# Kernel tuning notes

Hardware: AMD Instinct MI355X
Metric: run time of the kernel (lower is better)

The kernel has to match this reference:

```python
import jax, jax.numpy as jnp
import numpy as np

N_USER = 200000
N_ITEM = 200000
N_EDGE = 6400000
FEAT = 128
HID = 128
ALPHA = 0.1  # opt['leakey']


def _leaky(x):
    return jnp.where(x >= 0, x, ALPHA * x)


def setup_inputs() -> dict:
    key = jax.random.key(0)
    ks = jax.random.split(key, 16)
    s = 0.05
    return {
        "ufea": jax.random.normal(ks[0], (N_USER, FEAT), jnp.float32),
        "vfea": jax.random.normal(ks[1], (N_ITEM, FEAT), jnp.float32),
        "uv_rows": jax.random.randint(ks[2], (N_EDGE,), 0, N_USER, jnp.int32),
        "uv_cols": jax.random.randint(ks[3], (N_EDGE,), 0, N_ITEM, jnp.int32),
        "uv_vals": jax.random.uniform(ks[4], (N_EDGE,), jnp.float32),
        "vu_vals": jax.random.uniform(ks[5], (N_EDGE,), jnp.float32),
        "W1": jax.random.normal(ks[6], (FEAT, HID), jnp.float32) * s,
        "b1": jnp.zeros((HID,), jnp.float32),
        "W2": jax.random.normal(ks[7], (FEAT, HID), jnp.float32) * s,
        "b2": jnp.zeros((HID,), jnp.float32),
        "W3": jax.random.normal(ks[8], (HID, FEAT), jnp.float32) * s,
        "b3": jnp.zeros((FEAT,), jnp.float32),
        "W4": jax.random.normal(ks[9], (HID, FEAT), jnp.float32) * s,
        "b4": jnp.zeros((FEAT,), jnp.float32),
        "Wu": jax.random.normal(ks[10], (2 * FEAT, FEAT), jnp.float32) * s,
        "bu": jnp.zeros((FEAT,), jnp.float32),
        "Wi": jax.random.normal(ks[11], (2 * FEAT, FEAT), jnp.float32) * s,
        "bi": jnp.zeros((FEAT,), jnp.float32),
    }


def _spmm_u2i(vals, rows, cols, h):
    # VU_adj @ h : out[item] = sum_e vals[e] * h[rows[e]]
    return jax.ops.segment_sum(vals[:, None] * h[rows], cols, num_segments=N_ITEM)


def _spmm_i2u(vals, rows, cols, h):
    # UV_adj @ h : out[user] = sum_e vals[e] * h[cols[e]]
    return jax.ops.segment_sum(vals[:, None] * h[cols], rows, num_segments=N_USER)


def reference(ufea, vfea, uv_rows, uv_cols, uv_vals, vu_vals,
              W1, b1, W2, b2, W3, b3, W4, b4, Wu, bu, Wi, bi):
    # gc1: GCN(feat->hid) with VU_adj : users aggregated onto items
    user_ho = _leaky(_spmm_u2i(vu_vals, uv_rows, uv_cols, ufea @ W1) + b1)
    # gc2: GCN(feat->hid) with UV_adj : items aggregated onto users
    item_ho = _leaky(_spmm_i2u(uv_vals, uv_rows, uv_cols, vfea @ W2) + b2)
    # gc3: GCN(hid->feat) with UV_adj : back to user side
    user_ho = _leaky(_spmm_i2u(uv_vals, uv_rows, uv_cols, user_ho @ W3) + b3)
    # gc4: GCN(hid->feat) with VU_adj : back to item side
    item_ho = _leaky(_spmm_u2i(vu_vals, uv_rows, uv_cols, item_ho @ W4) + b4)
    user = jnp.concatenate([user_ho, ufea], axis=1) @ Wu + bu
    item = jnp.concatenate([item_ho, vfea], axis=1) @ Wi + bi
    return jax.nn.relu(user), jax.nn.relu(item)
```

## Files before the change

kernel.cpp:

```cpp
#include <hip/hip_runtime.h>

#define N_NODE 200000
#define FEAT 128
#define ALPHA 0.1f
#define NB 782
#define P2CAP 9216
#define VQ 16383.0f

typedef __bf16 bf16x8 __attribute__((ext_vector_type(8)));
typedef float  f32x4  __attribute__((ext_vector_type(4)));

__device__ inline unsigned short bf16r(float x) {
    unsigned u = __float_as_uint(x);
    u += ((u >> 16) & 1u) + 0x7FFFu;
    return (unsigned short)(u >> 16);
}
__device__ inline unsigned bf16pk(float a, float b) {
    unsigned ua = __float_as_uint(a); ua += ((ua >> 16) & 1u) + 0x7FFFu;
    unsigned ub = __float_as_uint(b); ub += ((ub >> 16) & 1u) + 0x7FFFu;
    return (ua >> 16) | (ub & 0xFFFF0000u);
}
__device__ inline bf16x8 cvt8(const float* __restrict__ p) {
    float4 a = *(const float4*)p, b = *(const float4*)(p + 4);
    union { bf16x8 v; unsigned short u[8]; } o;
    o.u[0] = bf16r(a.x); o.u[1] = bf16r(a.y); o.u[2] = bf16r(a.z); o.u[3] = bf16r(a.w);
    o.u[4] = bf16r(b.x); o.u[5] = bf16r(b.y); o.u[6] = bf16r(b.z); o.u[7] = bf16r(b.w);
    return o.v;
}

__global__ __launch_bounds__(512) void p0_hist(
        const int* __restrict__ rows, const int* __restrict__ cols,
        int* __restrict__ cntA, int* __restrict__ cntB, int nedge) {
    __shared__ int hA[NB], hB[NB];
    int t = threadIdx.x;
    for (int i = t; i < NB; i += 512) { hA[i] = 0; hB[i] = 0; }
    __syncthreads();
    int b0 = blockIdx.x * 16384;
    int bend = min(b0 + 16384, nedge);
    for (int e = b0 + t; e < bend; e += 512) {
        atomicAdd(&hA[cols[e] >> 8], 1);
        atomicAdd(&hB[rows[e] >> 8], 1);
    }
    __syncthreads();
    for (int i = t; i < NB; i += 512) {
        if (hA[i]) atomicAdd(&cntA[i], hA[i]);
        if (hB[i]) atomicAdd(&cntB[i], hB[i]);
    }
}

__global__ __launch_bounds__(1024) void scan2(
        const int* __restrict__ cntA, const int* __restrict__ cntB,
        int* __restrict__ bBaseA, int* __restrict__ bCurA,
        int* __restrict__ bBaseB, int* __restrict__ bCurB, int nedge) {
    __shared__ int s[1024];
    int t = threadIdx.x;
    for (int pass = 0; pass < 2; ++pass) {
        const int* cnt = pass ? cntB : cntA;
        int* bBase = pass ? bBaseB : bBaseA;
        int* bCur  = pass ? bCurB  : bCurA;
        int v = (t < NB) ? cnt[t] : 0;
        s[t] = v;
        __syncthreads();
        for (int o = 1; o < 1024; o <<= 1) {
            int a = (t >= o) ? s[t - o] : 0;
            __syncthreads();
            s[t] += a;
            __syncthreads();
        }
        int exc = s[t] - v;
        if (t < NB) { bBase[t] = exc; bCur[t] = exc; }
        if (t == 0) bBase[NB] = nedge;
        __syncthreads();
    }
}

#define BIN_E 32768
__global__ __launch_bounds__(512) void bin_dual(
        const int* __restrict__ rows, const int* __restrict__ cols,
        const float* __restrict__ uvv, const float* __restrict__ vuv,
        int* __restrict__ bCurA, int* __restrict__ bCurB,
        int2* __restrict__ sA, int2* __restrict__ sB, int nedge) {
    __shared__ int hA[NB], hB[NB], baA[NB], baB[NB], cuA[NB], cuB[NB];
    int t = threadIdx.x;
    for (int i = t; i < NB; i += 512) { hA[i] = 0; hB[i] = 0; }
    __syncthreads();
    int b0 = blockIdx.x * BIN_E;
    int bend = min(b0 + BIN_E, nedge);
    for (int e = b0 + t; e < bend; e += 512) {
        atomicAdd(&hA[cols[e] >> 8], 1);
        atomicAdd(&hB[rows[e] >> 8], 1);
    }
    __syncthreads();
    for (int i = t; i < NB; i += 512) {
        baA[i] = hA[i] ? atomicAdd(&bCurA[i], hA[i]) : 0;  cuA[i] = 0;
        baB[i] = hB[i] ? atomicAdd(&bCurB[i], hB[i]) : 0;  cuB[i] = 0;
    }
    __syncthreads();
    for (int e = b0 + t; e < bend; e += 512) {
        int r = rows[e], c = cols[e];
        int kA = c >> 8;
        int pA = baA[kA] + atomicAdd(&cuA[kA], 1);
        sA[pA] = make_int2(((c & 255) << 18) | r, __float_as_int(vuv[e]));
        int kB = r >> 8;
        int pB = baB[kB] + atomicAdd(&cuB[kB], 1);
        sB[pB] = make_int2(((r & 255) << 18) | c, __float_as_int(uvv[e]));
    }
}

__global__ __launch_bounds__(512) void p2_sort(
        const int2* __restrict__ sA, const int* __restrict__ bBaseA,
        unsigned* __restrict__ eA, int* __restrict__ rpA,
        const int2* __restrict__ sB, const int* __restrict__ bBaseB,
        unsigned* __restrict__ eB, int* __restrict__ rpB) {
    __shared__ unsigned sorted[P2CAP];
    __shared__ int c256[256], off[256];
    const int2* s; const int* bB; unsigned* e; int* rp;
    if (blockIdx.y == 0) { s = sA; bB = bBaseA; e = eA; rp = rpA; }
    else                 { s = sB; bB = bBaseB; e = eB; rp = rpB; }
    int k = blockIdx.x;
    int base = bB[k], end = bB[k + 1];
    int t = threadIdx.x;
    if (t < 256) c256[t] = 0;
    __syncthreads();
    for (int i = base + t; i < end; i += 512)
        atomicAdd(&c256[((unsigned)s[i].x) >> 18], 1);
    __syncthreads();
    int v = (t < 256) ? c256[t] : 0;
    if (t < 256) off[t] = v;
    __syncthreads();
    for (int o = 1; o < 256; o <<= 1) {
        int a = (t >= o && t < 256) ? off[t - o] : 0;
        __syncthreads();
        if (t < 256) off[t] += a;
        __syncthreads();
    }
    if (t < 256) {
        int exc = off[t] - v;
        off[t] = exc;
        c256[t] = 0;
        int node = (k << 8) + t;
        if (node < N_NODE) rp[node] = base + exc;
    }
    __syncthreads();
    for (int i = base + t; i < end; i += 512) {
        int2 rec = s[i];
        int loc = ((unsigned)rec.x) >> 18;
        int slot = off[loc] + atomicAdd(&c256[loc], 1);
        unsigned q = (unsigned)__float2int_rn(__int_as_float(rec.y) * VQ);
        if (slot < P2CAP)
            sorted[slot] = (((unsigned)rec.x & 0x3FFFFu) << 14) | q;
    }
    __syncthreads();
    int cnt = end - base;
    if (cnt > P2CAP) cnt = P2CAP;
    for (int i = t; i < cnt; i += 512)
        e[base + i] = sorted[i];
    if (k == NB - 1 && t == 0) rp[N_NODE] = bB[NB];
}

__global__ __launch_bounds__(256) void wtrans(
        const float* __restrict__ W, unsigned short* __restrict__ Wt, int K) {
    int idx = blockIdx.x * 256 + threadIdx.x;
    if (idx >= K * 128) return;
    int k = idx >> 7, n = idx & 127;
    Wt[n * K + k] = bf16r(W[idx]);
}

__global__ __launch_bounds__(256) void spmm_gather_act_bf16(
        const unsigned* __restrict__ src, unsigned* __restrict__ dst,
        const int* __restrict__ rp, const unsigned* __restrict__ edges,
        const float* __restrict__ bias, int ndst) {
    int wid = __builtin_amdgcn_readfirstlane(
        (int)((blockIdx.x * 256u + threadIdx.x) >> 6));
    int lane = threadIdx.x & 63;
    if (wid >= ndst) return;
    float2 b = *(const float2*)(bias + lane * 2);
    int e0 = rp[wid], e1 = rp[wid + 1];
    float accx = 0.f, accy = 0.f;
    const float vs = 1.0f / VQ;
    int e = e0;
    for (; e + 8 <= e1; e += 8) {
        unsigned r0 = edges[e],     r1 = edges[e + 1];
        unsigned r2 = edges[e + 2], r3 = edges[e + 3];
        unsigned r4 = edges[e + 4], r5 = edges[e + 5];
        unsigned r6 = edges[e + 6], r7 = edges[e + 7];
        unsigned p0 = src[(size_t)(r0 >> 14) * 64 + lane];
        unsigned p1 = src[(size_t)(r1 >> 14) * 64 + lane];
        unsigned p2 = src[(size_t)(r2 >> 14) * 64 + lane];
        unsigned p3 = src[(size_t)(r3 >> 14) * 64 + lane];
        unsigned p4 = src[(size_t)(r4 >> 14) * 64 + lane];
        unsigned p5 = src[(size_t)(r5 >> 14) * 64 + lane];
        unsigned p6 = src[(size_t)(r6 >> 14) * 64 + lane];
        unsigned p7 = src[(size_t)(r7 >> 14) * 64 + lane];
        float v0 = (float)(r0 & 16383u) * vs, v1 = (float)(r1 & 16383u) * vs;
        float v2 = (float)(r2 & 16383u) * vs, v3 = (float)(r3 & 16383u) * vs;
        float v4 = (float)(r4 & 16383u) * vs, v5 = (float)(r5 & 16383u) * vs;
        float v6 = (float)(r6 & 16383u) * vs, v7 = (float)(r7 & 16383u) * vs;
        accx = fmaf(v0, __uint_as_float(p0 << 16), accx);
        accy = fmaf(v0, __uint_as_float(p0 & 0xFFFF0000u), accy);
        accx = fmaf(v1, __uint_as_float(p1 << 16), accx);
        accy = fmaf(v1, __uint_as_float(p1 & 0xFFFF0000u), accy);
        accx = fmaf(v2, __uint_as_float(p2 << 16), accx);
        accy = fmaf(v2, __uint_as_float(p2 & 0xFFFF0000u), accy);
        accx = fmaf(v3, __uint_as_float(p3 << 16), accx);
        accy = fmaf(v3, __uint_as_float(p3 & 0xFFFF0000u), accy);
        accx = fmaf(v4, __uint_as_float(p4 << 16), accx);
        accy = fmaf(v4, __uint_as_float(p4 & 0xFFFF0000u), accy);
        accx = fmaf(v5, __uint_as_float(p5 << 16), accx);
        accy = fmaf(v5, __uint_as_float(p5 & 0xFFFF0000u), accy);
        accx = fmaf(v6, __uint_as_float(p6 << 16), accx);
        accy = fmaf(v6, __uint_as_float(p6 & 0xFFFF0000u), accy);
        accx = fmaf(v7, __uint_as_float(p7 << 16), accx);
        accy = fmaf(v7, __uint_as_float(p7 & 0xFFFF0000u), accy);
    }
    for (; e < e1; ++e) {
        unsigned r = edges[e];
        unsigned p = src[(size_t)(r >> 14) * 64 + lane];
        float v = (float)(r & 16383u) * vs;
        accx = fmaf(v, __uint_as_float(p << 16), accx);
        accy = fmaf(v, __uint_as_float(p & 0xFFFF0000u), accy);
    }
    float ox = accx + b.x;
    float oy = accy + b.y;
    ox = (ox >= 0.f) ? ox : ALPHA * ox;
    oy = (oy >= 0.f) ? oy : ALPHA * oy;
    dst[(size_t)wid * 64 + lane] = bf16pk(ox, oy);
}

__global__ __launch_bounds__(256) void gemm16(
        const unsigned short* __restrict__ X, const unsigned short* __restrict__ Wt,
        unsigned short* __restrict__ O, int M) {
    int l = threadIdx.x & 63, wv = threadIdx.x >> 6;
    int lr = l & 15, lh = l >> 4;
    int row0 = blockIdx.x * 128 + wv * 32;
    int ra = row0 + lr, rb = row0 + 16 + lr;
    if (ra >= M) ra = M - 1;
    if (rb >= M) rb = M - 1;
    const unsigned short* xa = X + (size_t)ra * 128;
    const unsigned short* xb = X + (size_t)rb * 128;
    f32x4 acc[2][8] = {};
#pragma unroll
    for (int ks = 0; ks < 4; ++ks) {
        int ko = ks * 32 + lh * 8;
        bf16x8 a0 = *(const bf16x8*)(xa + ko);
        bf16x8 a1 = *(const bf16x8*)(xb + ko);
#pragma unroll
        for (int nf = 0; nf < 8; ++nf) {
            bf16x8 b = *(const bf16x8*)(Wt + (nf * 16 + lr) * 128 + ko);
            acc[0][nf] = __builtin_amdgcn_mfma_f32_16x16x32_bf16(a0, b, acc[0][nf], 0, 0, 0);
            acc[1][nf] = __builtin_amdgcn_mfma_f32_16x16x32_bf16(a1, b, acc[1][nf], 0, 0, 0);
        }
    }
#pragma unroll
    for (int half = 0; half < 2; ++half) {
        int orow = row0 + half * 16 + lh * 4;
#pragma unroll
        for (int j = 0; j < 4; ++j) {
            if (orow + j < M) {
                unsigned short* op = O + (size_t)(orow + j) * 128 + lr;
#pragma unroll
                for (int nf = 0; nf < 8; ++nf)
                    op[nf * 16] = bf16r(acc[half][nf][j]);
            }
        }
    }
}

__global__ __launch_bounds__(256) void gemm16_f32(
        const float* __restrict__ Xf, const unsigned short* __restrict__ Wt,
        unsigned short* __restrict__ O, int M) {
    int l = threadIdx.x & 63, wv = threadIdx.x >> 6;
    int lr = l & 15, lh = l >> 4;
    int row0 = blockIdx.x * 128 + wv * 32;
    int ra = row0 + lr, rb = row0 + 16 + lr;
    if (ra >= M) ra = M - 1;
    if (rb >= M) rb = M - 1;
    const float* xa = Xf + (size_t)ra * 128;
    const float* xb = Xf + (size_t)rb * 128;
    f32x4 acc[2][8] = {};
#pragma unroll
    for (int ks = 0; ks < 4; ++ks) {
        int ko = ks * 32 + lh * 8;
        bf16x8 a0 = cvt8(xa + ko);
        bf16x8 a1 = cvt8(xb + ko);
#pragma unroll
        for (int nf = 0; nf < 8; ++nf) {
            bf16x8 b = *(const bf16x8*)(Wt + (nf * 16 + lr) * 128 + ko);
            acc[0][nf] = __builtin_amdgcn_mfma_f32_16x16x32_bf16(a0, b, acc[0][nf], 0, 0, 0);
            acc[1][nf] = __builtin_amdgcn_mfma_f32_16x16x32_bf16(a1, b, acc[1][nf], 0, 0, 0);
        }
    }
#pragma unroll
    for (int half = 0; half < 2; ++half) {
        int orow = row0 + half * 16 + lh * 4;
#pragma unroll
        for (int j = 0; j < 4; ++j) {
            if (orow + j < M) {
                unsigned short* op = O + (size_t)(orow + j) * 128 + lr;
#pragma unroll
                for (int nf = 0; nf < 8; ++nf)
                    op[nf * 16] = bf16r(acc[half][nf][j]);
            }
        }
    }
}

__global__ __launch_bounds__(256) void gemm16_concat(
        const unsigned short* __restrict__ T, const float* __restrict__ F,
        const unsigned short* __restrict__ Wt, const float* __restrict__ bias,
        float* __restrict__ O, int M) {
    int l = threadIdx.x & 63, wv = threadIdx.x >> 6;
    int lr = l & 15, lh = l >> 4;
    int row0 = blockIdx.x * 128 + wv * 32;
    int ra = row0 + lr, rb = row0 + 16 + lr;
    if (ra >= M) ra = M - 1;
    if (rb >= M) rb = M - 1;
    f32x4 acc[2][8] = {};
#pragma unroll
    for (int ks = 0; ks < 8; ++ks) {
        int ko = (ks & 3) * 32 + lh * 8;
        bf16x8 a0, a1;
        if (ks < 4) {
            a0 = *(const bf16x8*)(T + (size_t)ra * 128 + ko);
            a1 = *(const bf16x8*)(T + (size_t)rb * 128 + ko);
        } else {
            a0 = cvt8(F + (size_t)ra * 128 + ko);
            a1 = cvt8(F + (size_t)rb * 128 + ko);
        }
        int wko = ks * 32 + lh * 8;
#pragma unroll
        for (int nf = 0; nf < 8; ++nf) {
            bf16x8 b = *(const bf16x8*)(Wt + (nf * 16 + lr) * 256 + wko);
            acc[0][nf] = __builtin_amdgcn_mfma_f32_16x16x32_bf16(a0, b, acc[0][nf], 0, 0, 0);
            acc[1][nf] = __builtin_amdgcn_mfma_f32_16x16x32_bf16(a1, b, acc[1][nf], 0, 0, 0);
        }
    }
    float bv[8];
#pragma unroll
    for (int nf = 0; nf < 8; ++nf) bv[nf] = bias[nf * 16 + lr];
#pragma unroll
    for (int half = 0; half < 2; ++half) {
        int orow = row0 + half * 16 + lh * 4;
#pragma unroll
        for (int j = 0; j < 4; ++j) {
            if (orow + j < M) {
                float* op = O + (size_t)(orow + j) * 128 + lr;
#pragma unroll
                for (int nf = 0; nf < 8; ++nf) {
                    float v = acc[half][nf][j] + bv[nf];
                    op[nf * 16] = v > 0.f ? v : 0.f;
                }
            }
        }
    }
}

extern "C" void kernel_launch(void* const* d_in, const int* in_sizes, int n_in,
                              void* d_out, int out_size, void* d_ws, size_t ws_size,
                              hipStream_t stream) {
    const float* ufea    = (const float*)d_in[0];
    const float* vfea    = (const float*)d_in[1];
    const int*   uv_rows = (const int*)d_in[2];
    const int*   uv_cols = (const int*)d_in[3];
    const float* uv_vals = (const float*)d_in[4];
    const float* vu_vals = (const float*)d_in[5];
    const float* W1 = (const float*)d_in[6];
    const float* b1 = (const float*)d_in[7];
    const float* W2 = (const float*)d_in[8];
    const float* b2 = (const float*)d_in[9];
    const float* W3 = (const float*)d_in[10];
    const float* b3 = (const float*)d_in[11];
    const float* W4 = (const float*)d_in[12];
    const float* b4 = (const float*)d_in[13];
    const float* Wu = (const float*)d_in[14];
    const float* bu = (const float*)d_in[15];
    const float* Wi = (const float*)d_in[16];
    const float* bi = (const float*)d_in[17];

    float* out_user = (float*)d_out;
    float* out_item = out_user + (size_t)N_NODE * FEAT;

    int nedge = in_sizes[2];
    size_t nfe = (size_t)N_NODE * FEAT;

    unsigned short* G1 = (unsigned short*)d_ws;
    unsigned short* G2 = G1 + nfe;
    unsigned short* Ta = G2 + nfe;
    unsigned short* Tb = Ta + nfe;
    unsigned short* W1t = Tb + nfe;
    unsigned short* W2t = W1t + 128 * 128;
    unsigned short* W3t = W2t + 128 * 128;
    unsigned short* W4t = W3t + 128 * 128;
    unsigned short* Wut = W4t + 128 * 128;
    unsigned short* Wit = Wut + 128 * 256;
    int* rpA    = (int*)(Wit + 128 * 256);
    int* rpB    = rpA + (N_NODE + 64);
    int* cntA   = rpB + (N_NODE + 64);
    int* cntB   = cntA + 1024;
    int* bBaseA = cntB + 1024;
    int* bBaseB = bBaseA + 1024;
    int* bCurA  = bBaseB + 1024;
    int* bCurB  = bCurA + 1024;
    unsigned* eA = (unsigned*)(bCurB + 1024);
    unsigned* eB = eA + nedge;

    int2* sA = (int2*)G1;
    int2* sB = (int2*)G2;

    dim3 b512(512), b256(256);
    int hb  = (nedge + 16383) / 16384;
    int binb = (nedge + BIN_E - 1) / BIN_E;
    dim3 mgrid((unsigned)((N_NODE + 127) / 128));
    dim3 sgrid((unsigned)(N_NODE / 4));
    dim3 p2grid(NB, 2);

    hipMemsetAsync(cntA, 0, 2048 * sizeof(int), stream);
    p0_hist<<<hb, b512, 0, stream>>>(uv_rows, uv_cols, cntA, cntB, nedge);
    scan2<<<1, 1024, 0, stream>>>(cntA, cntB, bBaseA, bCurA, bBaseB, bCurB, nedge);
    bin_dual<<<binb, b512, 0, stream>>>(uv_rows, uv_cols, uv_vals, vu_vals,
                                        bCurA, bCurB, sA, sB, nedge);
    p2_sort<<<p2grid, b512, 0, stream>>>(sA, bBaseA, eA, rpA,
                                         sB, bBaseB, eB, rpB);

    wtrans<<<64, b256, 0, stream>>>(W1, W1t, 128);
    wtrans<<<64, b256, 0, stream>>>(W2, W2t, 128);
    wtrans<<<64, b256, 0, stream>>>(W3, W3t, 128);
    wtrans<<<64, b256, 0, stream>>>(W4, W4t, 128);
    wtrans<<<128, b256, 0, stream>>>(Wu, Wut, 256);
    wtrans<<<128, b256, 0, stream>>>(Wi, Wit, 256);

    gemm16_f32<<<mgrid, b256, 0, stream>>>(ufea, W1t, G1, N_NODE);
    spmm_gather_act_bf16<<<sgrid, b256, 0, stream>>>(
        (const unsigned*)G1, (unsigned*)Ta, rpA, eA, b1, N_NODE);

    gemm16_f32<<<mgrid, b256, 0, stream>>>(vfea, W2t, G2, N_NODE);
    spmm_gather_act_bf16<<<sgrid, b256, 0, stream>>>(
        (const unsigned*)G2, (unsigned*)Tb, rpB, eB, b2, N_NODE);

    gemm16<<<mgrid, b256, 0, stream>>>(Ta, W3t, G1, N_NODE);
    spmm_gather_act_bf16<<<sgrid, b256, 0, stream>>>(
        (const unsigned*)G1, (unsigned*)Ta, rpB, eB, b3, N_NODE);

    gemm16<<<mgrid, b256, 0, stream>>>(Tb, W4t, G2, N_NODE);
    spmm_gather_act_bf16<<<sgrid, b256, 0, stream>>>(
        (const unsigned*)G2, (unsigned*)Tb, rpA, eA, b4, N_NODE);

    gemm16_concat<<<mgrid, b256, 0, stream>>>(Ta, ufea, Wut, bu, out_user, N_NODE);
    gemm16_concat<<<mgrid, b256, 0, stream>>>(Tb, vfea, Wit, bi, out_item, N_NODE);
}
```

Before: 1.600 ms.

## Fuse per-bucket local sort into SpMM gather, dropping CSR build pass

Removes the separate p2_sort kernel and the compact CSR edge arrays. Each SpMM launch now loads its bucket's binned records, counting-sorts them in shared memory and immediately does the weighted gather with bias and leaky ReLU. Binned records get dedicated workspace, and the binning kernel switches to a fixed count of 128 blocks. This saves a global write and read of sorted edges, but repeats the sort in every SpMM, reads wider records, and runs far fewer, longer-lived waves.

Result: slower. 1.761 ms (+10.1%).

```diff
diff --git a/kernel.cpp b/kernel.cpp
--- a/kernel.cpp
+++ b/kernel.cpp
@@ -4,7 +4,7 @@
 #define FEAT 128
 #define ALPHA 0.1f
 #define NB 782
-#define P2CAP 9216
+#define GCAP 9216
 #define VQ 16383.0f
 
 typedef __bf16 bf16x8 __attribute__((ext_vector_type(8)));
@@ -74,18 +74,18 @@
     }
 }
 
-#define BIN_E 32768
 __global__ __launch_bounds__(512) void bin_dual(
         const int* __restrict__ rows, const int* __restrict__ cols,
         const float* __restrict__ uvv, const float* __restrict__ vuv,
         int* __restrict__ bCurA, int* __restrict__ bCurB,
-        int2* __restrict__ sA, int2* __restrict__ sB, int nedge) {
+        int2* __restrict__ sA, int2* __restrict__ sB,
+        int nedge, int chunk) {
     __shared__ int hA[NB], hB[NB], baA[NB], baB[NB], cuA[NB], cuB[NB];
     int t = threadIdx.x;
     for (int i = t; i < NB; i += 512) { hA[i] = 0; hB[i] = 0; }
     __syncthreads();
-    int b0 = blockIdx.x * BIN_E;
-    int bend = min(b0 + BIN_E, nedge);
+    int b0 = blockIdx.x * chunk;
+    int bend = min(b0 + chunk, nedge);
     for (int e = b0 + t; e < bend; e += 512) {
         atomicAdd(&hA[cols[e] >> 8], 1);
         atomicAdd(&hB[rows[e] >> 8], 1);
@@ -107,25 +107,21 @@
     }
 }
 
-__global__ __launch_bounds__(512) void p2_sort(
-        const int2* __restrict__ sA, const int* __restrict__ bBaseA,
-        unsigned* __restrict__ eA, int* __restrict__ rpA,
-        const int2* __restrict__ sB, const int* __restrict__ bBaseB,
-        unsigned* __restrict__ eB, int* __restrict__ rpB) {
-    __shared__ unsigned sorted[P2CAP];
-    __shared__ int c256[256], off[256];
-    const int2* s; const int* bB; unsigned* e; int* rp;
-    if (blockIdx.y == 0) { s = sA; bB = bBaseA; e = eA; rp = rpA; }
-    else                 { s = sB; bB = bBaseB; e = eB; rp = rpB; }
+__global__ __launch_bounds__(512) void bucket_gather(
+        const int2* __restrict__ recs, const int* __restrict__ bBase,
+        const unsigned* __restrict__ G, unsigned* __restrict__ dstF,
+        const float* __restrict__ bias) {
+    __shared__ unsigned sorted[GCAP];
+    __shared__ int cnt[256], off[256];
     int k = blockIdx.x;
-    int base = bB[k], end = bB[k + 1];
+    int base = bBase[k], end = bBase[k + 1];
     int t = threadIdx.x;
-    if (t < 256) c256[t] = 0;
+    if (t < 256) cnt[t] = 0;
     __syncthreads();
     for (int i = base + t; i < end; i += 512)
-        atomicAdd(&c256[((unsigned)s[i].x) >> 18], 1);
-    __syncthreads();
-    int v = (t < 256) ? c256[t] : 0;
+        atomicAdd(&cnt[((unsigned)recs[i].x) >> 18], 1);
+    __syncthreads();
+    int v = (t < 256) ? cnt[t] : 0;
     if (t < 256) off[t] = v;
     __syncthreads();
     for (int o = 1; o < 256; o <<= 1) {
@@ -134,28 +130,61 @@
         if (t < 256) off[t] += a;
         __syncthreads();
     }
-    if (t < 256) {
-        int exc = off[t] - v;
-        off[t] = exc;
-        c256[t] = 0;
-        int node = (k << 8) + t;
-        if (node < N_NODE) rp[node] = base + exc;
-    }
+    if (t < 256) { off[t] -= v; cnt[t] = 0; }
     __syncthreads();
     for (int i = base + t; i < end; i += 512) {
-        int2 rec = s[i];
-        int loc = ((unsigned)rec.x) >> 18;
-        int slot = off[loc] + atomicAdd(&c256[loc], 1);
-        unsigned q = (unsigned)__float2int_rn(__int_as_float(rec.y) * VQ);
-        if (slot < P2CAP)
-            sorted[slot] = (((unsigned)rec.x & 0x3FFFFu) << 14) | q;
-    }
-    __syncthreads();
-    int cnt = end - base;
-    if (cnt > P2CAP) cnt = P2CAP;
-    for (int i = t; i < cnt; i += 512)
-        e[base + i] = sorted[i];
-    if (k == NB - 1 && t == 0) rp[N_NODE] = bB[NB];
+        int2 r = recs[i];
+        int loc = ((unsigned)r.x) >> 18;
+        int slot = off[loc] + atomicAdd(&cnt[loc], 1);
+        unsigned q = (unsigned)__float2int_rn(__int_as_float(r.y) * VQ);
+        if (slot < GCAP)
+            sorted[slot] = ((((unsigned)r.x) & 0x3FFFFu) << 14) | q;
+    }
+    __syncthreads();
+
+    int wave = t >> 6, lane = t & 63;
+    float2 bb = *(const float2*)(bias + lane * 2);
+    const float vs = 1.0f / VQ;
+    for (int j = 0; j < 32; ++j) {
+        int loc = (wave << 5) + j;
+        int node = (k << 8) + loc;
+        if (node >= N_NODE) break;
+        int e0 = off[loc];
+        int e1 = e0 + cnt[loc];
+        if (e1 > GCAP) e1 = GCAP;
+        float ax = 0.f, ay = 0.f;
+        int e = e0;
+        for (; e + 4 <= e1; e += 4) {
+            unsigned r0 = sorted[e],     r1 = sorted[e + 1];
+            unsigned r2 = sorted[e + 2], r3 = sorted[e + 3];
+            unsigned p0 = G[(size_t)(r0 >> 14) * 64 + lane];
+            unsigned p1 = G[(size_t)(r1 >> 14) * 64 + lane];
+            unsigned p2 = G[(size_t)(r2 >> 14) * 64 + lane];
+            unsigned p3 = G[(size_t)(r3 >> 14) * 64 + lane];
+            float v0 = (float)(r0 & 16383u) * vs, v1 = (float)(r1 & 16383u) * vs;
+            float v2 = (float)(r2 & 16383u) * vs, v3 = (float)(r3 & 16383u) * vs;
+            ax = fmaf(v0, __uint_as_float(p0 << 16), ax);
+            ay = fmaf(v0, __uint_as_float(p0 & 0xFFFF0000u), ay);
+            ax = fmaf(v1, __uint_as_float(p1 << 16), ax);
+            ay = fmaf(v1, __uint_as_float(p1 & 0xFFFF0000u), ay);
+            ax = fmaf(v2, __uint_as_float(p2 << 16), ax);
+            ay = fmaf(v2, __uint_as_float(p2 & 0xFFFF0000u), ay);
+            ax = fmaf(v3, __uint_as_float(p3 << 16), ax);
+            ay = fmaf(v3, __uint_as_float(p3 & 0xFFFF0000u), ay);
+        }
+        for (; e < e1; ++e) {
+            unsigned r = sorted[e];
+            unsigned p = G[(size_t)(r >> 14) * 64 + lane];
+            float vv = (float)(r & 16383u) * vs;
+            ax = fmaf(vv, __uint_as_float(p << 16), ax);
+            ay = fmaf(vv, __uint_as_float(p & 0xFFFF0000u), ay);
+        }
+        float ox = ax + bb.x;
+        float oy = ay + bb.y;
+        ox = (ox >= 0.f) ? ox : ALPHA * ox;
+        oy = (oy >= 0.f) ? oy : ALPHA * oy;
+        dstF[(size_t)node * 64 + lane] = bf16pk(ox, oy);
+    }
 }
 
 __global__ __launch_bounds__(256) void wtrans(
@@ -164,67 +193,6 @@
     if (idx >= K * 128) return;
     int k = idx >> 7, n = idx & 127;
     Wt[n * K + k] = bf16r(W[idx]);
-}
-
-__global__ __launch_bounds__(256) void spmm_gather_act_bf16(
-        const unsigned* __restrict__ src, unsigned* __restrict__ dst,
-        const int* __restrict__ rp, const unsigned* __restrict__ edges,
-        const float* __restrict__ bias, int ndst) {
-    int wid = __builtin_amdgcn_readfirstlane(
-        (int)((blockIdx.x * 256u + threadIdx.x) >> 6));
-    int lane = threadIdx.x & 63;
-    if (wid >= ndst) return;
-    float2 b = *(const float2*)(bias + lane * 2);
-    int e0 = rp[wid], e1 = rp[wid + 1];
-    float accx = 0.f, accy = 0.f;
-    const float vs = 1.0f / VQ;
-    int e = e0;
-    for (; e + 8 <= e1; e += 8) {
-        unsigned r0 = edges[e],     r1 = edges[e + 1];
-        unsigned r2 = edges[e + 2], r3 = edges[e + 3];
-        unsigned r4 = edges[e + 4], r5 = edges[e + 5];
-        unsigned r6 = edges[e + 6], r7 = edges[e + 7];
-        unsigned p0 = src[(size_t)(r0 >> 14) * 64 + lane];
-        unsigned p1 = src[(size_t)(r1 >> 14) * 64 + lane];
-        unsigned p2 = src[(size_t)(r2 >> 14) * 64 + lane];
-        unsigned p3 = src[(size_t)(r3 >> 14) * 64 + lane];
-        unsigned p4 = src[(size_t)(r4 >> 14) * 64 + lane];
-        unsigned p5 = src[(size_t)(r5 >> 14) * 64 + lane];
-        unsigned p6 = src[(size_t)(r6 >> 14) * 64 + lane];
-        unsigned p7 = src[(size_t)(r7 >> 14) * 64 + lane];
-        float v0 = (float)(r0 & 16383u) * vs, v1 = (float)(r1 & 16383u) * vs;
-        float v2 = (float)(r2 & 16383u) * vs, v3 = (float)(r3 & 16383u) * vs;
-        float v4 = (float)(r4 & 16383u) * vs, v5 = (float)(r5 & 16383u) * vs;
-        float v6 = (float)(r6 & 16383u) * vs, v7 = (float)(r7 & 16383u) * vs;
-        accx = fmaf(v0, __uint_as_float(p0 << 16), accx);
-        accy = fmaf(v0, __uint_as_float(p0 & 0xFFFF0000u), accy);
-        accx = fmaf(v1, __uint_as_float(p1 << 16), accx);
-        accy = fmaf(v1, __uint_as_float(p1 & 0xFFFF0000u), accy);
-        accx = fmaf(v2, __uint_as_float(p2 << 16), accx);
-        accy = fmaf(v2, __uint_as_float(p2 & 0xFFFF0000u), accy);
-        accx = fmaf(v3, __uint_as_float(p3 << 16), accx);
-        accy = fmaf(v3, __uint_as_float(p3 & 0xFFFF0000u), accy);
-        accx = fmaf(v4, __uint_as_float(p4 << 16), accx);
-        accy = fmaf(v4, __uint_as_float(p4 & 0xFFFF0000u), accy);
-        accx = fmaf(v5, __uint_as_float(p5 << 16), accx);
-        accy = fmaf(v5, __uint_as_float(p5 & 0xFFFF0000u), accy);
-        accx = fmaf(v6, __uint_as_float(p6 << 16), accx);
-        accy = fmaf(v6, __uint_as_float(p6 & 0xFFFF0000u), accy);
-        accx = fmaf(v7, __uint_as_float(p7 << 16), accx);
-        accy = fmaf(v7, __uint_as_float(p7 & 0xFFFF0000u), accy);
-    }
-    for (; e < e1; ++e) {
-        unsigned r = edges[e];
-        unsigned p = src[(size_t)(r >> 14) * 64 + lane];
-        float v = (float)(r & 16383u) * vs;
-        accx = fmaf(v, __uint_as_float(p << 16), accx);
-        accy = fmaf(v, __uint_as_float(p & 0xFFFF0000u), accy);
-    }
-    float ox = accx + b.x;
-    float oy = accy + b.y;
-    ox = (ox >= 0.f) ? ox : ALPHA * ox;
-    oy = (oy >= 0.f) ? oy : ALPHA * oy;
-    dst[(size_t)wid * 64 + lane] = bf16pk(ox, oy);
 }
 
 __global__ __launch_bounds__(256) void gemm16(
@@ -387,40 +355,33 @@
     unsigned short* G2 = G1 + nfe;
     unsigned short* Ta = G2 + nfe;
     unsigned short* Tb = Ta + nfe;
-    unsigned short* W1t = Tb + nfe;
+    int2* sA = (int2*)(Tb + nfe);
+    int2* sB = sA + nedge;
+    unsigned short* W1t = (unsigned short*)(sB + nedge);
     unsigned short* W2t = W1t + 128 * 128;
     unsigned short* W3t = W2t + 128 * 128;
     unsigned short* W4t = W3t + 128 * 128;
     unsigned short* Wut = W4t + 128 * 128;
     unsigned short* Wit = Wut + 128 * 256;
-    int* rpA    = (int*)(Wit + 128 * 256);
-    int* rpB    = rpA + (N_NODE + 64);
-    int* cntA   = rpB + (N_NODE + 64);
+    int* cntA   = (int*)(Wit + 128 * 256);
     int* cntB   = cntA + 1024;
     int* bBaseA = cntB + 1024;
     int* bBaseB = bBaseA + 1024;
     int* bCurA  = bBaseB + 1024;
     int* bCurB  = bCurA + 1024;
-    unsigned* eA = (unsigned*)(bCurB + 1024);
-    unsigned* eB = eA + nedge;
-
-    int2* sA = (int2*)G1;
-    int2* sB = (int2*)G2;
 
     dim3 b512(512), b256(256);
-    int hb  = (nedge + 16383) / 16384;
-    int binb = (nedge + BIN_E - 1) / BIN_E;
+    int hb = (nedge + 16383) / 16384;
+    int binb = 128;
+    int chunk = (nedge + binb - 1) / binb;
     dim3 mgrid((unsigned)((N_NODE + 127) / 128));
-    dim3 sgrid((unsigned)(N_NODE / 4));
-    dim3 p2grid(NB, 2);
+    dim3 bggrid(NB);
 
     hipMemsetAsync(cntA, 0, 2048 * sizeof(int), stream);
     p0_hist<<<hb, b512, 0, stream>>>(uv_rows, uv_cols, cntA, cntB, nedge);
     scan2<<<1, 1024, 0, stream>>>(cntA, cntB, bBaseA, bCurA, bBaseB, bCurB, nedge);
     bin_dual<<<binb, b512, 0, stream>>>(uv_rows, uv_cols, uv_vals, vu_vals,
-                                        bCurA, bCurB, sA, sB, nedge);
-    p2_sort<<<p2grid, b512, 0, stream>>>(sA, bBaseA, eA, rpA,
-                                         sB, bBaseB, eB, rpB);
+                                        bCurA, bCurB, sA, sB, nedge, chunk);
 
     wtrans<<<64, b256, 0, stream>>>(W1, W1t, 128);
     wtrans<<<64, b256, 0, stream>>>(W2, W2t, 128);
@@ -430,20 +391,20 @@
     wtrans<<<128, b256, 0, stream>>>(Wi, Wit, 256);
 
     gemm16_f32<<<mgrid, b256, 0, stream>>>(ufea, W1t, G1, N_NODE);
-    spmm_gather_act_bf16<<<sgrid, b256, 0, stream>>>(
-        (const unsigned*)G1, (unsigned*)Ta, rpA, eA, b1, N_NODE);
+    bucket_gather<<<bggrid, b512, 0, stream>>>(sA, bBaseA, (const unsigned*)G1,
+                                               (unsigned*)Ta, b1);
 
     gemm16_f32<<<mgrid, b256, 0, stream>>>(vfea, W2t, G2, N_NODE);
-    spmm_gather_act_bf16<<<sgrid, b256, 0, stream>>>(
-        (const unsigned*)G2, (unsigned*)Tb, rpB, eB, b2, N_NODE);
+    bucket_gather<<<bggrid, b512, 0, stream>>>(sB, bBaseB, (const unsigned*)G2,
+                                               (unsigned*)Tb, b2);
 
     gemm16<<<mgrid, b256, 0, stream>>>(Ta, W3t, G1, N_NODE);
-    spmm_gather_act_bf16<<<sgrid, b256, 0, stream>>>(
-        (const unsigned*)G1, (unsigned*)Ta, rpB, eB, b3, N_NODE);
+    bucket_gather<<<bggrid, b512, 0, stream>>>(sB, bBaseB, (const unsigned*)G1,
+                                               (unsigned*)Ta, b3);
 
     gemm16<<<mgrid, b256, 0, stream>>>(Tb, W4t, G2, N_NODE);
-    spmm_gather_act_bf16<<<sgrid, b256, 0, stream>>>(
-        (const unsigned*)G2, (unsigned*)Tb, rpA, eA, b4, N_NODE);
+    bucket_gather<<<bggrid, b512, 0, stream>>>(sA, bBaseA, (const unsigned*)G2,
+                                               (unsigned*)Tb, b4);
 
     gemm16_concat<<<mgrid, b256, 0, stream>>>(Ta, ufea, Wut, bu, out_user, N_NODE);
     gemm16_concat<<<mgrid, b256, 0, stream>>>(Tb, vfea, Wit, bi, out_item, N_NODE);
```

## Split edge binning into two-level radix passes, fuse weight and concat launches

Applied to the files above, without the earlier changes.

Edge binning used to scatter straight into 782 fine buckets. It now scatters first into 25 coarse super-buckets and then, in a second pass, into 32 sub-buckets each. This is meant to make the scattered writes more coherent and cut global atomics, at the cost of one extra read and write pass over the edge records. The six weight-transpose launches are merged into one, as are the two final concat GEMMs. Nontemporal loads and stores are added on streamed edge and output data, and the workspace is re-laid out so the edge arrays alias the feature buffers.

New measurement: 1.521 ms. 4.9% less time.

```diff
diff --git a/kernel.cpp b/kernel.cpp
--- a/kernel.cpp
+++ b/kernel.cpp
@@ -4,16 +4,18 @@
 #define FEAT 128
 #define ALPHA 0.1f
 #define NB 782
+#define SBN 25
 #define P2CAP 9216
 #define VQ 16383.0f
 
 typedef __bf16 bf16x8 __attribute__((ext_vector_type(8)));
 typedef float  f32x4  __attribute__((ext_vector_type(4)));
-
-__device__ inline unsigned short bf16r(float x) {
+typedef unsigned short ushort_t;
+
+__device__ inline ushort_t bf16r(float x) {
     unsigned u = __float_as_uint(x);
     u += ((u >> 16) & 1u) + 0x7FFFu;
-    return (unsigned short)(u >> 16);
+    return (ushort_t)(u >> 16);
 }
 __device__ inline unsigned bf16pk(float a, float b) {
     unsigned ua = __float_as_uint(a); ua += ((ua >> 16) & 1u) + 0x7FFFu;
@@ -22,7 +24,7 @@
 }
 __device__ inline bf16x8 cvt8(const float* __restrict__ p) {
     float4 a = *(const float4*)p, b = *(const float4*)(p + 4);
-    union { bf16x8 v; unsigned short u[8]; } o;
+    union { bf16x8 v; ushort_t u[8]; } o;
     o.u[0] = bf16r(a.x); o.u[1] = bf16r(a.y); o.u[2] = bf16r(a.z); o.u[3] = bf16r(a.w);
     o.u[4] = bf16r(b.x); o.u[5] = bf16r(b.y); o.u[6] = bf16r(b.z); o.u[7] = bf16r(b.w);
     return o.v;
@@ -48,16 +50,20 @@
     }
 }
 
-__global__ __launch_bounds__(1024) void scan2(
+__global__ __launch_bounds__(1024) void scan_all(
         const int* __restrict__ cntA, const int* __restrict__ cntB,
         int* __restrict__ bBaseA, int* __restrict__ bCurA,
-        int* __restrict__ bBaseB, int* __restrict__ bCurB, int nedge) {
+        int* __restrict__ sbaseA, int* __restrict__ sCurA,
+        int* __restrict__ bBaseB, int* __restrict__ bCurB,
+        int* __restrict__ sbaseB, int* __restrict__ sCurB, int nedge) {
     __shared__ int s[1024];
     int t = threadIdx.x;
     for (int pass = 0; pass < 2; ++pass) {
         const int* cnt = pass ? cntB : cntA;
         int* bBase = pass ? bBaseB : bBaseA;
         int* bCur  = pass ? bCurB  : bCurA;
+        int* sbase = pass ? sbaseB : sbaseA;
+        int* sCur  = pass ? sCurB  : sCurA;
         int v = (t < NB) ? cnt[t] : 0;
         s[t] = v;
         __syncthreads();
@@ -68,62 +74,106 @@
             __syncthreads();
         }
         int exc = s[t] - v;
-        if (t < NB) { bBase[t] = exc; bCur[t] = exc; }
-        if (t == 0) bBase[NB] = nedge;
+        if (t < NB) {
+            bBase[t] = exc;
+            bCur[t] = exc;
+            if ((t & 31) == 0) { sbase[t >> 5] = exc; sCur[t >> 5] = exc; }
+        }
+        if (t == 0) { bBase[NB] = nedge; sbase[SBN] = nedge; }
         __syncthreads();
     }
 }
 
-#define BIN_E 32768
-__global__ __launch_bounds__(512) void bin_dual(
+__global__ __launch_bounds__(512) void passA_bin(
         const int* __restrict__ rows, const int* __restrict__ cols,
         const float* __restrict__ uvv, const float* __restrict__ vuv,
-        int* __restrict__ bCurA, int* __restrict__ bCurB,
-        int2* __restrict__ sA, int2* __restrict__ sB, int nedge) {
-    __shared__ int hA[NB], hB[NB], baA[NB], baB[NB], cuA[NB], cuB[NB];
+        int* __restrict__ sCurA, int* __restrict__ sCurB,
+        int2* __restrict__ iA, int2* __restrict__ iB, int nedge) {
+    __shared__ int hA[SBN], hB[SBN], bA[SBN], bB[SBN], cA[SBN], cB[SBN];
     int t = threadIdx.x;
-    for (int i = t; i < NB; i += 512) { hA[i] = 0; hB[i] = 0; }
-    __syncthreads();
-    int b0 = blockIdx.x * BIN_E;
-    int bend = min(b0 + BIN_E, nedge);
+    if (t < SBN) { hA[t] = 0; hB[t] = 0; }
+    __syncthreads();
+    int b0 = blockIdx.x * 16384;
+    int bend = min(b0 + 16384, nedge);
     for (int e = b0 + t; e < bend; e += 512) {
-        atomicAdd(&hA[cols[e] >> 8], 1);
-        atomicAdd(&hB[rows[e] >> 8], 1);
-    }
-    __syncthreads();
-    for (int i = t; i < NB; i += 512) {
-        baA[i] = hA[i] ? atomicAdd(&bCurA[i], hA[i]) : 0;  cuA[i] = 0;
-        baB[i] = hB[i] ? atomicAdd(&bCurB[i], hB[i]) : 0;  cuB[i] = 0;
+        atomicAdd(&hA[cols[e] >> 13], 1);
+        atomicAdd(&hB[rows[e] >> 13], 1);
+    }
+    __syncthreads();
+    if (t < SBN) {
+        bA[t] = hA[t] ? atomicAdd(&sCurA[t], hA[t]) : 0;  cA[t] = 0;
+        bB[t] = hB[t] ? atomicAdd(&sCurB[t], hB[t]) : 0;  cB[t] = 0;
     }
     __syncthreads();
     for (int e = b0 + t; e < bend; e += 512) {
         int r = rows[e], c = cols[e];
-        int kA = c >> 8;
-        int pA = baA[kA] + atomicAdd(&cuA[kA], 1);
-        sA[pA] = make_int2(((c & 255) << 18) | r, __float_as_int(vuv[e]));
-        int kB = r >> 8;
-        int pB = baB[kB] + atomicAdd(&cuB[kB], 1);
-        sB[pB] = make_int2(((r & 255) << 18) | c, __float_as_int(uvv[e]));
+        float vu = __builtin_nontemporal_load(vuv + e);
+        float uv = __builtin_nontemporal_load(uvv + e);
+        int sA = c >> 13;
+        int pA = bA[sA] + atomicAdd(&cA[sA], 1);
+        iA[pA] = make_int2(((c & 8191) << 18) | r, __float_as_int(vu));
+        int sB = r >> 13;
+        int pB = bB[sB] + atomicAdd(&cB[sB], 1);
+        iB[pB] = make_int2(((r & 8191) << 18) | c, __float_as_int(uv));
+    }
+}
+
+__global__ __launch_bounds__(512) void passB_bin(
+        const int2* __restrict__ iA, int2* __restrict__ fA,
+        const int* __restrict__ sbaseA, int* __restrict__ bCurA,
+        const int2* __restrict__ iB, int2* __restrict__ fB,
+        const int* __restrict__ sbaseB, int* __restrict__ bCurB) {
+    __shared__ int h[32], base_[32], cur[32];
+    const int2* iX; int2* fX; const int* sbase; int* bCur;
+    if (blockIdx.z == 0) { iX = iA; fX = fA; sbase = sbaseA; bCur = bCurA; }
+    else                 { iX = iB; fX = fB; sbase = sbaseB; bCur = bCurB; }
+    int sb = blockIdx.y;
+    int i0 = sbase[sb] + blockIdx.x * 16384;
+    int iend = sbase[sb + 1];
+    if (i0 >= iend) return;
+    if (iend > i0 + 16384) iend = i0 + 16384;
+
+    int t = threadIdx.x;
+    if (t < 32) h[t] = 0;
+    __syncthreads();
+    for (int i = i0 + t; i < iend; i += 512) {
+        unsigned x = (unsigned)__builtin_nontemporal_load(&iX[i].x);
+        atomicAdd(&h[(x >> 26) & 31], 1);
+    }
+    __syncthreads();
+    if (t < 32) {
+        base_[t] = h[t] ? atomicAdd(&bCur[sb * 32 + t], h[t]) : 0;
+        cur[t] = 0;
+    }
+    __syncthreads();
+    for (int i = i0 + t; i < iend; i += 512) {
+        long long raw = __builtin_nontemporal_load((const long long*)(iX + i));
+        int2 rec = make_int2((int)(raw & 0xFFFFFFFFll), (int)(raw >> 32));
+        int b = (((unsigned)rec.x) >> 26) & 31;
+        int p = base_[b] + atomicAdd(&cur[b], 1);
+        fX[p] = rec;
     }
 }
 
 __global__ __launch_bounds__(512) void p2_sort(
-        const int2* __restrict__ sA, const int* __restrict__ bBaseA,
+        const int2* __restrict__ fA, const int* __restrict__ bBaseA,
         unsigned* __restrict__ eA, int* __restrict__ rpA,
-        const int2* __restrict__ sB, const int* __restrict__ bBaseB,
+        const int2* __restrict__ fB, const int* __restrict__ bBaseB,
         unsigned* __restrict__ eB, int* __restrict__ rpB) {
     __shared__ unsigned sorted[P2CAP];
     __shared__ int c256[256], off[256];
     const int2* s; const int* bB; unsigned* e; int* rp;
-    if (blockIdx.y == 0) { s = sA; bB = bBaseA; e = eA; rp = rpA; }
-    else                 { s = sB; bB = bBaseB; e = eB; rp = rpB; }
+    if (blockIdx.y == 0) { s = fA; bB = bBaseA; e = eA; rp = rpA; }
+    else                 { s = fB; bB = bBaseB; e = eB; rp = rpB; }
     int k = blockIdx.x;
     int base = bB[k], end = bB[k + 1];
     int t = threadIdx.x;
     if (t < 256) c256[t] = 0;
     __syncthreads();
-    for (int i = base + t; i < end; i += 512)
-        atomicAdd(&c256[((unsigned)s[i].x) >> 18], 1);
+    for (int i = base + t; i < end; i += 512) {
+        unsigned x = (unsigned)__builtin_nontemporal_load(&s[i].x);
+        atomicAdd(&c256[(x >> 18) & 255], 1);
+    }
     __syncthreads();
     int v = (t < 256) ? c256[t] : 0;
     if (t < 256) off[t] = v;
@@ -143,12 +193,13 @@
     }
     __syncthreads();
     for (int i = base + t; i < end; i += 512) {
-        int2 rec = s[i];
-        int loc = ((unsigned)rec.x) >> 18;
+        long long raw = __builtin_nontemporal_load((const long long*)(s + i));
+        int2 rec = make_int2((int)(raw & 0xFFFFFFFFll), (int)(raw >> 32));
+        int loc = (((unsigned)rec.x) >> 18) & 255;
         int slot = off[loc] + atomicAdd(&c256[loc], 1);
         unsigned q = (unsigned)__float2int_rn(__int_as_float(rec.y) * VQ);
         if (slot < P2CAP)
-            sorted[slot] = (((unsigned)rec.x & 0x3FFFFu) << 14) | q;
+            sorted[slot] = ((((unsigned)rec.x) & 0x3FFFFu) << 14) | q;
     }
     __syncthreads();
     int cnt = end - base;
@@ -158,8 +209,22 @@
     if (k == NB - 1 && t == 0) rp[N_NODE] = bB[NB];
 }
 
-__global__ __launch_bounds__(256) void wtrans(
-        const float* __restrict__ W, unsigned short* __restrict__ Wt, int K) {
+__global__ __launch_bounds__(256) void wtrans_all(
+        const float* __restrict__ W1, const float* __restrict__ W2,
+        const float* __restrict__ W3, const float* __restrict__ W4,
+        const float* __restrict__ Wu, const float* __restrict__ Wi,
+        ushort_t* __restrict__ W1t, ushort_t* __restrict__ W2t,
+        ushort_t* __restrict__ W3t, ushort_t* __restrict__ W4t,
+        ushort_t* __restrict__ Wut, ushort_t* __restrict__ Wit) {
+    const float* W; ushort_t* Wt; int K;
+    switch (blockIdx.y) {
+        case 0: W = W1; Wt = W1t; K = 128; break;
+        case 1: W = W2; Wt = W2t; K = 128; break;
+        case 2: W = W3; Wt = W3t; K = 128; break;
+        case 3: W = W4; Wt = W4t; K = 128; break;
+        case 4: W = Wu; Wt = Wut; K = 256; break;
+        default: W = Wi; Wt = Wit; K = 256; break;
+    }
     int idx = blockIdx.x * 256 + threadIdx.x;
     if (idx >= K * 128) return;
     int k = idx >> 7, n = idx & 127;
@@ -180,10 +245,14 @@
     const float vs = 1.0f / VQ;
     int e = e0;
     for (; e + 8 <= e1; e += 8) {
-        unsigned r0 = edges[e],     r1 = edges[e + 1];
-        unsigned r2 = edges[e + 2], r3 = edges[e + 3];
-        unsigned r4 = edges[e + 4], r5 = edges[e + 5];
-        unsigned r6 = edges[e + 6], r7 = edges[e + 7];
+        unsigned r0 = __builtin_nontemporal_load(edges + e);
+        unsigned r1 = __builtin_nontemporal_load(edges + e + 1);
+        unsigned r2 = __builtin_nontemporal_load(edges + e + 2);
+        unsigned r3 = __builtin_nontemporal_load(edges + e + 3);
+        unsigned r4 = __builtin_nontemporal_load(edges + e + 4);
+        unsigned r5 = __builtin_nontemporal_load(edges + e + 5);
+        unsigned r6 = __builtin_nontemporal_load(edges + e + 6);
+        unsigned r7 = __builtin_nontemporal_load(edges + e + 7);
         unsigned p0 = src[(size_t)(r0 >> 14) * 64 + lane];
         unsigned p1 = src[(size_t)(r1 >> 14) * 64 + lane];
         unsigned p2 = src[(size_t)(r2 >> 14) * 64 + lane];
@@ -214,7 +283,7 @@
         accy = fmaf(v7, __uint_as_float(p7 & 0xFFFF0000u), accy);
     }
     for (; e < e1; ++e) {
-        unsigned r = edges[e];
+        unsigned r = __builtin_nontemporal_load(edges + e);
         unsigned p = src[(size_t)(r >> 14) * 64 + lane];
         float v = (float)(r & 16383u) * vs;
         accx = fmaf(v, __uint_as_float(p << 16), accx);
@@ -224,20 +293,20 @@
     float oy = accy + b.y;
     ox = (ox >= 0.f) ? ox : ALPHA * ox;
     oy = (oy >= 0.f) ? oy : ALPHA * oy;
-    dst[(size_t)wid * 64 + lane] = bf16pk(ox, oy);
+    __builtin_nontemporal_store(bf16pk(ox, oy), dst + (size_t)wid * 64 + lane);
 }
 
 __global__ __launch_bounds__(256) void gemm16(
-        const unsigned short* __restrict__ X, const unsigned short* __restrict__ Wt,
-        unsigned short* __restrict__ O, int M) {
+        const ushort_t* __restrict__ X, const ushort_t* __restrict__ Wt,
+        ushort_t* __restrict__ O, int M) {
     int l = threadIdx.x & 63, wv = threadIdx.x >> 6;
     int lr = l & 15, lh = l >> 4;
     int row0 = blockIdx.x * 128 + wv * 32;
     int ra = row0 + lr, rb = row0 + 16 + lr;
     if (ra >= M) ra = M - 1;
     if (rb >= M) rb = M - 1;
-    const unsigned short* xa = X + (size_t)ra * 128;
-    const unsigned short* xb = X + (size_t)rb * 128;
+    const ushort_t* xa = X + (size_t)ra * 128;
+    const ushort_t* xb = X + (size_t)rb * 128;
     f32x4 acc[2][8] = {};
 #pragma unroll
     for (int ks = 0; ks < 4; ++ks) {
@@ -257,7 +326,7 @@
 #pragma unroll
         for (int j = 0; j < 4; ++j) {
             if (orow + j < M) {
-                unsigned short* op = O + (size_t)(orow + j) * 128 + lr;
+                ushort_t* op = O + (size_t)(orow + j) * 128 + lr;
 #pragma unroll
                 for (int nf = 0; nf < 8; ++nf)
                     op[nf * 16] = bf16r(acc[half][nf][j]);
@@ -267,8 +336,8 @@
 }
 
 __global__ __launch_bounds__(256) void gemm16_f32(
-        const float* __restrict__ Xf, const unsigned short* __restrict__ Wt,
-        unsigned short* __restrict__ O, int M) {
+        const float* __restrict__ Xf, const ushort_t* __restrict__ Wt,
+        ushort_t* __restrict__ O, int M) {
     int l = threadIdx.x & 63, wv = threadIdx.x >> 6;
     int lr = l & 15, lh = l >> 4;
     int row0 = blockIdx.x * 128 + wv * 32;
@@ -296,7 +365,7 @@
 #pragma unroll
         for (int j = 0; j < 4; ++j) {
             if (orow + j < M) {
-                unsigned short* op = O + (size_t)(orow + j) * 128 + lr;
+                ushort_t* op = O + (size_t)(orow + j) * 128 + lr;
 #pragma unroll
                 for (int nf = 0; nf < 8; ++nf)
                     op[nf * 16] = bf16r(acc[half][nf][j]);
@@ -305,10 +374,17 @@
     }
 }
 
-__global__ __launch_bounds__(256) void gemm16_concat(
-        const unsigned short* __restrict__ T, const float* __restrict__ F,
-        const unsigned short* __restrict__ Wt, const float* __restrict__ bias,
-        float* __restrict__ O, int M) {
+__global__ __launch_bounds__(256) void concat_dual(
+        const ushort_t* __restrict__ TA, const float* __restrict__ FA,
+        const ushort_t* __restrict__ WtA, const float* __restrict__ bA,
+        float* __restrict__ OA,
+        const ushort_t* __restrict__ TB, const float* __restrict__ FB,
+        const ushort_t* __restrict__ WtB, const float* __restrict__ bB,
+        float* __restrict__ OB, int M) {
+    const ushort_t* T; const float* F; const ushort_t* Wt; const float* bias;
+    float* O;
+    if (blockIdx.y == 0) { T = TA; F = FA; Wt = WtA; bias = bA; O = OA; }
+    else                 { T = TB; F = FB; Wt = WtB; bias = bB; O = OB; }
     int l = threadIdx.x & 63, wv = threadIdx.x >> 6;
     int lr = l & 15, lh = l >> 4;
     int row0 = blockIdx.x * 128 + wv * 32;
@@ -348,7 +424,7 @@
 #pragma unroll
                 for (int nf = 0; nf < 8; ++nf) {
                     float v = acc[half][nf][j] + bv[nf];
-                    op[nf * 16] = v > 0.f ? v : 0.f;
+                    __builtin_nontemporal_store(v > 0.f ? v : 0.f, op + nf * 16);
                 }
             }
         }
@@ -383,16 +459,18 @@
     int nedge = in_sizes[2];
     size_t nfe = (size_t)N_NODE * FEAT;
 
-    unsigned short* G1 = (unsigned short*)d_ws;
-    unsigned short* G2 = G1 + nfe;
-    unsigned short* Ta = G2 + nfe;
-    unsigned short* Tb = Ta + nfe;
-    unsigned short* W1t = Tb + nfe;
-    unsigned short* W2t = W1t + 128 * 128;
-    unsigned short* W3t = W2t + 128 * 128;
-    unsigned short* W4t = W3t + 128 * 128;
-    unsigned short* Wut = W4t + 128 * 128;
-    unsigned short* Wit = Wut + 128 * 256;
+    int2* iA = (int2*)d_ws;
+    int2* iB = iA + nedge;
+    int2* fA = iB + nedge;
+    int2* fB = fA + nedge;
+    unsigned* eA32 = (unsigned*)(fB + nedge);
+    unsigned* eB32 = eA32 + nedge;
+    ushort_t* W1t = (ushort_t*)(eB32 + nedge);
+    ushort_t* W2t = W1t + 128 * 128;
+    ushort_t* W3t = W2t + 128 * 128;
+    ushort_t* W4t = W3t + 128 * 128;
+    ushort_t* Wut = W4t + 128 * 128;
+    ushort_t* Wit = Wut + 128 * 256;
     int* rpA    = (int*)(Wit + 128 * 256);
     int* rpB    = rpA + (N_NODE + 64);
     int* cntA   = rpB + (N_NODE + 64);
@@ -401,50 +479,56 @@
     int* bBaseB = bBaseA + 1024;
     int* bCurA  = bBaseB + 1024;
     int* bCurB  = bCurA + 1024;
-    unsigned* eA = (unsigned*)(bCurB + 1024);
-    unsigned* eB = eA + nedge;
-
-    int2* sA = (int2*)G1;
-    int2* sB = (int2*)G2;
+    int* sbaseA = bCurB + 1024;
+    int* sbaseB = sbaseA + 64;
+    int* sCurA  = sbaseB + 64;
+    int* sCurB  = sCurA + 64;
+
+    ushort_t* G1 = (ushort_t*)iA;
+    ushort_t* G2 = (ushort_t*)iB;
+    ushort_t* Ta = (ushort_t*)fA;
+    ushort_t* Tb = (ushort_t*)fB;
 
     dim3 b512(512), b256(256);
-    int hb  = (nedge + 16383) / 16384;
-    int binb = (nedge + BIN_E - 1) / BIN_E;
+    int hb = (nedge + 16383) / 16384;
     dim3 mgrid((unsigned)((N_NODE + 127) / 128));
     dim3 sgrid((unsigned)(N_NODE / 4));
+    dim3 pBgrid(17, SBN, 2);
     dim3 p2grid(NB, 2);
+    dim3 wgrid(128, 6);
+    dim3 cgrid((unsigned)((N_NODE + 127) / 128), 2);
+
+    wtrans_all<<<wgrid, b256, 0, stream>>>(W1, W2, W3, W4, Wu, Wi,
+                                           W1t, W2t, W3t, W4t, Wut, Wit);
 
     hipMemsetAsync(cntA, 0, 2048 * sizeof(int), stream);
     p0_hist<<<hb, b512, 0, stream>>>(uv_rows, uv_cols, cntA, cntB, nedge);
-    scan2<<<1, 1024, 0, stream>>>(cntA, cntB, bBaseA, bCurA, bBaseB, bCurB, nedge);
-    bin_dual<<<binb, b512, 0, stream>>>(uv_rows, uv_cols, uv_vals, vu_vals,
-                                        bCurA, bCurB, sA, sB, nedge);
-    p2_sort<<<p2grid, b512, 0, stream>>>(sA, bBaseA, eA, rpA,
-                                         sB, bBaseB, eB, rpB);
-
-    wtrans<<<64, b256, 0, stream>>>(W1, W1t, 128);
-    wtrans<<<64, b256, 0, stream>>>(W2, W2t, 128);
-    wtrans<<<64, b256, 0, stream>>>(W3, W3t, 128);
-    wtrans<<<64, b256, 0, stream>>>(W4, W4t, 128);
-    wtrans<<<128, b256, 0, stream>>>(Wu, Wut, 256);
-    wtrans<<<128, b256, 0, stream>>>(Wi, Wit, 256);
+    scan_all<<<1, 1024, 0, stream>>>(cntA, cntB,
+                                     bBaseA, bCurA, sbaseA, sCurA,
+                                     bBaseB, bCurB, sbaseB, sCurB, nedge);
+    passA_bin<<<hb, b512, 0, stream>>>(uv_rows, uv_cols, uv_vals, vu_vals,
+                                       sCurA, sCurB, iA, iB, nedge);
+    passB_bin<<<pBgrid, b512, 0, stream>>>(iA, fA, sbaseA, bCurA,
+                                           iB, fB, sbaseB, bCurB);
+    p2_sort<<<p2grid, b512, 0, stream>>>(fA, bBaseA, eA32, rpA,
+                                         fB, bBaseB, eB32, rpB);
 
     gemm16_f32<<<mgrid, b256, 0, stream>>>(ufea, W1t, G1, N_NODE);
     spmm_gather_act_bf16<<<sgrid, b256, 0, stream>>>(
-        (const unsigned*)G1, (unsigned*)Ta, rpA, eA, b1, N_NODE);
+        (const unsigned*)G1, (unsigned*)Ta, rpA, eA32, b1, N_NODE);
 
     gemm16_f32<<<mgrid, b256, 0, stream>>>(vfea, W2t, G2, N_NODE);
     spmm_gather_act_bf16<<<sgrid, b256, 0, stream>>>(
-        (const unsigned*)G2, (unsigned*)Tb, rpB, eB, b2, N_NODE);
+        (const unsigned*)G2, (unsigned*)Tb, rpB, eB32, b2, N_NODE);
 
     gemm16<<<mgrid, b256, 0, stream>>>(Ta, W3t, G1, N_NODE);
     spmm_gather_act_bf16<<<sgrid, b256, 0, stream>>>(
-        (const unsigned*)G1, (unsigned*)Ta, rpB, eB, b3, N_NODE);
+        (const unsigned*)G1, (unsigned*)Ta, rpB, eB32, b3, N_NODE);
 
     gemm16<<<mgrid, b256, 0, stream>>>(Tb, W4t, G2, N_NODE);
     spmm_gather_act_bf16<<<sgrid, b256, 0, stream>>>(
-        (const unsigned*)G2, (unsigned*)Tb, rpA, eA, b4, N_NODE);
-
-    gemm16_concat<<<mgrid, b256, 0, stream>>>(Ta, ufea, Wut, bu, out_user, N_NODE);
-    gemm16_concat<<<mgrid, b256, 0, stream>>>(Tb, vfea, Wit, bi, out_item, N_NODE);
-}
+        (const unsigned*)G2, (unsigned*)Tb, rpA, eA32, b4, N_NODE);
+
+    concat_dual<<<cgrid, b256, 0, stream>>>(Ta, ufea, Wut, bu, out_user,
+                                            Tb, vfea, Wit, bi, out_item, N_NODE);
+}
```
